# Kernel optimization log

Hardware: AMD Instinct MI355X
Metric: run time of the kernel (lower is better)

Reference implementation:

```python
import jax, jax.numpy as jnp
import numpy as np


def _pairwise_sq_dist(a, b):
    # a: (B,N,D), b: (B,M,D) -> (B,N,M) squared euclidean distances
    # matmul trick matching torch.cdist (clamped at 0 before implicit sqrt)
    a2 = jnp.sum(a * a, axis=-1)  # (B,N)
    b2 = jnp.sum(b * b, axis=-1)  # (B,M)
    ab = jnp.einsum('bnd,bmd->bnm', a, b)  # (B,N,M)
    d2 = a2[:, :, None] + b2[:, None, :] - 2.0 * ab
    return jnp.maximum(d2, 0.0)


def setup_inputs() -> dict:
    key = jax.random.key(0)
    k1, k2 = jax.random.split(key)
    B, N, M, D = 8, 8192, 8192, 3
    gts = jax.random.normal(k1, (B, N, D), dtype=jnp.float32)
    preds = jax.random.normal(k2, (B, M, D), dtype=jnp.float32)
    return {"gts": gts, "preds": preds}


def reference(gts, preds):
    d2 = _pairwise_sq_dist(gts, preds)           # (B,N,M)
    min_g2p = jnp.min(d2, axis=2)                # (B,N) nearest pred for each gt
    min_p2g = jnp.min(d2, axis=1)                # (B,M) nearest gt for each pred
    return jnp.mean(min_g2p) + jnp.mean(min_p2g)
```

## Files before the change

kernel.cpp:

```cpp
#include <hip/hip_runtime.h>
#include <math.h>

#define BB 8
#define NN 8192
#define MM 8192

#define ROWS_PER_BLOCK 256
#define COLS_PER_BLOCK 1024
#define NTILES (COLS_PER_BLOCK / 32)

typedef __attribute__((ext_vector_type(8)))  short short8;
typedef __attribute__((ext_vector_type(16))) float float16;

#define ONE_BF16 ((short)0x3F80)

__device__ inline unsigned short bf16rn(float f) {
    unsigned int u = __float_as_uint(f);
    u += 0x7FFFu + ((u >> 16) & 1u);
    return (unsigned short)(u >> 16);
}
__device__ inline float bf2f(unsigned short h) {
    return __uint_as_float(((unsigned int)h) << 16);
}
__device__ inline float min16(const float16 d) {
    float v = fminf(fminf(d[0], d[1]), d[2]);
    v = fminf(fminf(v, d[3]),  d[4]);
    v = fminf(fminf(v, d[5]),  d[6]);
    v = fminf(fminf(v, d[7]),  d[8]);
    v = fminf(fminf(v, d[9]),  d[10]);
    v = fminf(fminf(v, d[11]), d[12]);
    v = fminf(fminf(v, d[13]), d[14]);
    return fminf(v, d[15]);
}


__global__ __launch_bounds__(512, 4) void chamfer_main(
    const float* __restrict__ gts, const float* __restrict__ preds,
    unsigned int* __restrict__ minn, unsigned int* __restrict__ minp)
{
    __shared__ short8 sBlo[COLS_PER_BLOCK];
    __shared__ short8 sBhi[COLS_PER_BLOCK];
    __shared__ int colmin[COLS_PER_BLOCK];

    const int b       = blockIdx.z;
    const int rowBase = blockIdx.x * ROWS_PER_BLOCK;
    const int colBase = blockIdx.y * COLS_PER_BLOCK;
    const int tid  = threadIdx.x;
    const int lane = tid & 63;
    const int wave = tid >> 6;
    const int h    = lane >> 5;
    const int c    = lane & 31;

    for (int i = tid; i < COLS_PER_BLOCK; i += 512) {
        const float* p = preds + ((size_t)b * MM + colBase + i) * 3;
        float x = p[0], y = p[1], z = p[2];
        float w = x * x + y * y + z * z;
        unsigned short xh = bf16rn(x), yh = bf16rn(y), zh = bf16rn(z);
        unsigned short xl = bf16rn(x - bf2f(xh));
        unsigned short yl = bf16rn(y - bf2f(yh));
        unsigned short zl = bf16rn(z - bf2f(zh));
        unsigned short wh = bf16rn(w);
        unsigned short wl = bf16rn(w - bf2f(wh));
        short8 lo, hi;
        lo[0]=(short)xh; lo[1]=(short)yh; lo[2]=(short)zh; lo[3]=(short)xl;
        lo[4]=(short)yl; lo[5]=(short)zl; lo[6]=(short)xh; lo[7]=(short)yh;
        hi[0]=(short)zh; hi[1]=ONE_BF16;  hi[2]=ONE_BF16;  hi[3]=(short)wh;
        hi[4]=(short)wl; hi[5]=0;         hi[6]=0;         hi[7]=0;
        sBlo[i] = lo; sBhi[i] = hi;
        colmin[i] = 0x7F800000;
    }

    const float* g = gts + ((size_t)b * NN + rowBase + wave * 32 + c) * 3;
    float gx = g[0], gy = g[1], gz = g[2];
    float gw = gx * gx + gy * gy + gz * gz;
    float mx = -2.0f * gx, my = -2.0f * gy, mz = -2.0f * gz;
    unsigned short axh = bf16rn(mx), ayh = bf16rn(my), azh = bf16rn(mz);
    unsigned short axl = bf16rn(mx - bf2f(axh));
    unsigned short ayl = bf16rn(my - bf2f(ayh));
    unsigned short azl = bf16rn(mz - bf2f(azh));
    unsigned short awh = bf16rn(gw);
    unsigned short awl = bf16rn(gw - bf2f(awh));
    short8 alo, ahi;
    alo[0]=(short)axh; alo[1]=(short)ayh; alo[2]=(short)azh; alo[3]=(short)axh;
    alo[4]=(short)ayh; alo[5]=(short)azh; alo[6]=(short)axl; alo[7]=(short)ayl;
    ahi[0]=(short)azl; ahi[1]=(short)awh; ahi[2]=(short)awl; ahi[3]=ONE_BF16;
    ahi[4]=ONE_BF16;   ahi[5]=0;          ahi[6]=0;          ahi[7]=0;
    short8 afrag = h ? ahi : alo;

    float16 zacc;
#pragma unroll
    for (int q = 0; q < 16; ++q) zacc[q] = 0.0f;

    const float kInf = __builtin_inff();
    float rm[16];
#pragma unroll
    for (int q = 0; q < 16; ++q) rm[q] = kInf;

    __syncthreads();

    const short8* myB = h ? sBhi : sBlo;
    for (int t = 0; t < NTILES; t += 2) {
        short8 b0 = myB[t * 32 + c];
        short8 b1 = myB[(t + 1) * 32 + c];
        float16 d0 = __builtin_amdgcn_mfma_f32_32x32x16_bf16(afrag, b0, zacc, 0, 0, 0);
        float16 d1 = __builtin_amdgcn_mfma_f32_32x32x16_bf16(afrag, b1, zacc, 0, 0, 0);
        atomicMin(&colmin[t * 32 + c],       __float_as_int(min16(d0)));
        atomicMin(&colmin[(t + 1) * 32 + c], __float_as_int(min16(d1)));
#pragma unroll
        for (int q = 0; q < 16; ++q)
            rm[q] = fminf(fminf(rm[q], d0[q]), d1[q]);
    }

#pragma unroll
    for (int q = 0; q < 16; ++q) {
        float v = rm[q];
        v = fminf(v, __shfl_xor(v, 1));
        v = fminf(v, __shfl_xor(v, 2));
        v = fminf(v, __shfl_xor(v, 4));
        v = fminf(v, __shfl_xor(v, 8));
        v = fminf(v, __shfl_xor(v, 16));
        rm[q] = v;
    }
    float sel = rm[0];
#pragma unroll
    for (int q = 1; q < 16; ++q) sel = (c == q) ? rm[q] : sel;
    if (c < 16) {
        int rowInTile = (c & 3) + 8 * (c >> 2) + 4 * h;
        unsigned int bits = __float_as_uint(fmaxf(sel, 0.0f));
        atomicMin(&minn[(size_t)b * NN + rowBase + wave * 32 + rowInTile], bits);
    }

    __syncthreads();
    for (int i = tid; i < COLS_PER_BLOCK; i += 512) {
        unsigned int bits = __float_as_uint(fmaxf(__int_as_float(colmin[i]), 0.0f));
        atomicMin(&minp[(size_t)b * MM + colBase + i], bits);
    }
}

__global__ void chamfer_reduce(const unsigned int* __restrict__ minn,
                               const unsigned int* __restrict__ minp,
                               float* __restrict__ accum,
                               unsigned int* __restrict__ ticket,
                               float* __restrict__ out)
{
    const int idx = blockIdx.x * blockDim.x + threadIdx.x;
    const int stride = gridDim.x * blockDim.x;

    float s0 = 0.0f, s1 = 0.0f;
    for (int i = idx; i < BB * NN; i += stride) s0 += __uint_as_float(minn[i]);
    for (int i = idx; i < BB * MM; i += stride) s1 += __uint_as_float(minp[i]);

#pragma unroll
    for (int m = 1; m < 64; m <<= 1) {
        s0 += __shfl_xor(s0, m, 64);
        s1 += __shfl_xor(s1, m, 64);
    }
    __shared__ float w0[4], w1[4];
    if ((threadIdx.x & 63) == 0) {
        w0[threadIdx.x >> 6] = s0;
        w1[threadIdx.x >> 6] = s1;
    }
    __syncthreads();
    if (threadIdx.x == 0) {
        atomicAdd(&accum[0], w0[0] + w0[1] + w0[2] + w0[3]);
        atomicAdd(&accum[1], w1[0] + w1[1] + w1[2] + w1[3]);
        __threadfence();
        unsigned int old = atomicAdd(ticket, 1u);
        unsigned int G = gridDim.x;
        if (old == 0xAAAAAAAAu + G - 1u || old == G - 1u) {
            float a0 = atomicAdd(&accum[0], 0.0f);
            float a1 = atomicAdd(&accum[1], 0.0f);
            out[0] = a0 / (float)(BB * NN) + a1 / (float)(BB * MM);
        }
    }
}

extern "C" void kernel_launch(void* const* d_in, const int* in_sizes, int n_in,
                              void* d_out, int out_size, void* d_ws, size_t ws_size,
                              hipStream_t stream) {
    const float* gts   = (const float*)d_in[0];
    const float* preds = (const float*)d_in[1];
    float* out = (float*)d_out;

    unsigned int* minn   = (unsigned int*)d_ws;
    unsigned int* minp   = minn + (size_t)BB * NN;
    float*        accum  = (float*)(minp + (size_t)BB * MM);
    unsigned int* ticket = (unsigned int*)(accum + 2);

    dim3 grid(NN / ROWS_PER_BLOCK, MM / COLS_PER_BLOCK, BB);
    chamfer_main<<<grid, 512, 0, stream>>>(gts, preds, minn, minp);

    chamfer_reduce<<<64, 256, 0, stream>>>(minn, minp, accum, ticket, out);
}
```

Baseline: 93.80 us.

## Fuse chamfer into one kernel computing both directions as row-min passes

```diff
diff --git a/kernel.cpp b/kernel.cpp
--- a/kernel.cpp
+++ b/kernel.cpp
@@ -2,12 +2,7 @@
 #include <math.h>
 
 #define BB 8
-#define NN 8192
-#define MM 8192
-
-#define ROWS_PER_BLOCK 256
-#define COLS_PER_BLOCK 1024
-#define NTILES (COLS_PER_BLOCK / 32)
+#define PTS 8192
 
 typedef __attribute__((ext_vector_type(8)))  short short8;
 typedef __attribute__((ext_vector_type(16))) float float16;
@@ -22,155 +17,115 @@
 __device__ inline float bf2f(unsigned short h) {
     return __uint_as_float(((unsigned int)h) << 16);
 }
-__device__ inline float min16(const float16 d) {
-    float v = fminf(fminf(d[0], d[1]), d[2]);
-    v = fminf(fminf(v, d[3]),  d[4]);
-    v = fminf(fminf(v, d[5]),  d[6]);
-    v = fminf(fminf(v, d[7]),  d[8]);
-    v = fminf(fminf(v, d[9]),  d[10]);
-    v = fminf(fminf(v, d[11]), d[12]);
-    v = fminf(fminf(v, d[13]), d[14]);
-    return fminf(v, d[15]);
-}
 
+__global__ __launch_bounds__(512, 2) void chamfer_fused(
+    const float* __restrict__ gts, const float* __restrict__ preds,
+    float* __restrict__ accum, unsigned int* __restrict__ ticket,
+    float* __restrict__ out)
+{
+    __shared__ short8 sBlo[512];
+    __shared__ short8 sBhi[512];
 
-__global__ __launch_bounds__(512, 4) void chamfer_main(
-    const float* __restrict__ gts, const float* __restrict__ preds,
-    unsigned int* __restrict__ minn, unsigned int* __restrict__ minp)
-{
-    __shared__ short8 sBlo[COLS_PER_BLOCK];
-    __shared__ short8 sBhi[COLS_PER_BLOCK];
-    __shared__ int colmin[COLS_PER_BLOCK];
-
-    const int b       = blockIdx.z;
-    const int rowBase = blockIdx.x * ROWS_PER_BLOCK;
-    const int colBase = blockIdx.y * COLS_PER_BLOCK;
+    const int id     = blockIdx.x;
+    const int role   = id >> 8;
+    const int within = id & 255;
+    const int batch  = within >> 5;
+    const int qblk   = within & 31;
     const int tid  = threadIdx.x;
     const int lane = tid & 63;
     const int wave = tid >> 6;
     const int h    = lane >> 5;
     const int c    = lane & 31;
 
-    for (int i = tid; i < COLS_PER_BLOCK; i += 512) {
-        const float* p = preds + ((size_t)b * MM + colBase + i) * 3;
-        float x = p[0], y = p[1], z = p[2];
-        float w = x * x + y * y + z * z;
-        unsigned short xh = bf16rn(x), yh = bf16rn(y), zh = bf16rn(z);
-        unsigned short xl = bf16rn(x - bf2f(xh));
-        unsigned short yl = bf16rn(y - bf2f(yh));
-        unsigned short zl = bf16rn(z - bf2f(zh));
-        unsigned short wh = bf16rn(w);
-        unsigned short wl = bf16rn(w - bf2f(wh));
-        short8 lo, hi;
-        lo[0]=(short)xh; lo[1]=(short)yh; lo[2]=(short)zh; lo[3]=(short)xl;
-        lo[4]=(short)yl; lo[5]=(short)zl; lo[6]=(short)xh; lo[7]=(short)yh;
-        hi[0]=(short)zh; hi[1]=ONE_BF16;  hi[2]=ONE_BF16;  hi[3]=(short)wh;
-        hi[4]=(short)wl; hi[5]=0;         hi[6]=0;         hi[7]=0;
-        sBlo[i] = lo; sBhi[i] = hi;
-        colmin[i] = 0x7F800000;
-    }
+    const float* Q  = role ? preds : gts;
+    const float* DB = role ? gts : preds;
 
-    const float* g = gts + ((size_t)b * NN + rowBase + wave * 32 + c) * 3;
-    float gx = g[0], gy = g[1], gz = g[2];
-    float gw = gx * gx + gy * gy + gz * gz;
-    float mx = -2.0f * gx, my = -2.0f * gy, mz = -2.0f * gz;
-    unsigned short axh = bf16rn(mx), ayh = bf16rn(my), azh = bf16rn(mz);
-    unsigned short axl = bf16rn(mx - bf2f(axh));
-    unsigned short ayl = bf16rn(my - bf2f(ayh));
-    unsigned short azl = bf16rn(mz - bf2f(azh));
-    unsigned short awh = bf16rn(gw);
-    unsigned short awl = bf16rn(gw - bf2f(awh));
+    const float* q = Q + ((size_t)batch * PTS + qblk * 256 + wave * 32 + c) * 3;
+    float qx = q[0], qy = q[1], qz = q[2];
+    float wa = qx * qx + qy * qy + qz * qz;
+    float mX = -2.0f * qx, mY = -2.0f * qy, mZ = -2.0f * qz;
+    unsigned short mxh = bf16rn(mX), myh = bf16rn(mY), mzh = bf16rn(mZ);
+    unsigned short mxl = bf16rn(mX - bf2f(mxh));
+    unsigned short myl = bf16rn(mY - bf2f(myh));
+    unsigned short mzl = bf16rn(mZ - bf2f(mzh));
+    unsigned short awh = bf16rn(wa);
+    unsigned short awl = bf16rn(wa - bf2f(awh));
     short8 alo, ahi;
-    alo[0]=(short)axh; alo[1]=(short)ayh; alo[2]=(short)azh; alo[3]=(short)axh;
-    alo[4]=(short)ayh; alo[5]=(short)azh; alo[6]=(short)axl; alo[7]=(short)ayl;
-    ahi[0]=(short)azl; ahi[1]=(short)awh; ahi[2]=(short)awl; ahi[3]=ONE_BF16;
-    ahi[4]=ONE_BF16;   ahi[5]=0;          ahi[6]=0;          ahi[7]=0;
+    alo[0]=(short)mxh; alo[1]=(short)myh; alo[2]=(short)mzh; alo[3]=(short)mxh;
+    alo[4]=(short)myh; alo[5]=(short)mzh; alo[6]=(short)mxl; alo[7]=(short)myl;
+    ahi[0]=(short)mzl; ahi[1]=(short)mxl; ahi[2]=(short)myl; ahi[3]=(short)mzl;
+    ahi[4]=(short)awh; ahi[5]=(short)awl; ahi[6]=ONE_BF16;   ahi[7]=ONE_BF16;
     short8 afrag = h ? ahi : alo;
 
     float16 zacc;
 #pragma unroll
-    for (int q = 0; q < 16; ++q) zacc[q] = 0.0f;
+    for (int i = 0; i < 16; ++i) zacc[i] = 0.0f;
 
     const float kInf = __builtin_inff();
     float rm[16];
 #pragma unroll
-    for (int q = 0; q < 16; ++q) rm[q] = kInf;
+    for (int i = 0; i < 16; ++i) rm[i] = kInf;
 
-    __syncthreads();
+    const float* dbase = DB + (size_t)batch * PTS * 3;
 
-    const short8* myB = h ? sBhi : sBlo;
-    for (int t = 0; t < NTILES; t += 2) {
-        short8 b0 = myB[t * 32 + c];
-        short8 b1 = myB[(t + 1) * 32 + c];
-        float16 d0 = __builtin_amdgcn_mfma_f32_32x32x16_bf16(afrag, b0, zacc, 0, 0, 0);
-        float16 d1 = __builtin_amdgcn_mfma_f32_32x32x16_bf16(afrag, b1, zacc, 0, 0, 0);
-        atomicMin(&colmin[t * 32 + c],       __float_as_int(min16(d0)));
-        atomicMin(&colmin[(t + 1) * 32 + c], __float_as_int(min16(d1)));
+    for (int ch = 0; ch < PTS; ch += 512) {
+        __syncthreads();
+        {
+            const float* p = dbase + (size_t)(ch + tid) * 3;
+            float x = p[0], y = p[1], z = p[2];
+            float w = x * x + y * y + z * z;
+            unsigned short xh = bf16rn(x), yh = bf16rn(y), zh = bf16rn(z);
+            unsigned short xl = bf16rn(x - bf2f(xh));
+            unsigned short yl = bf16rn(y - bf2f(yh));
+            unsigned short zl = bf16rn(z - bf2f(zh));
+            unsigned short wh = bf16rn(w);
+            unsigned short wl = bf16rn(w - bf2f(wh));
+            short8 lo, hi;
+            lo[0]=(short)xh; lo[1]=(short)yh; lo[2]=(short)zh; lo[3]=(short)xl;
+            lo[4]=(short)yl; lo[5]=(short)zl; lo[6]=(short)xh; lo[7]=(short)yh;
+            hi[0]=(short)zh; hi[1]=(short)xl; hi[2]=(short)yl; hi[3]=(short)zl;
+            hi[4]=ONE_BF16;  hi[5]=ONE_BF16;  hi[6]=(short)wh; hi[7]=(short)wl;
+            sBlo[tid] = lo; sBhi[tid] = hi;
+        }
+        __syncthreads();
+
+        const short8* myB = h ? sBhi : sBlo;
 #pragma unroll
-        for (int q = 0; q < 16; ++q)
-            rm[q] = fminf(fminf(rm[q], d0[q]), d1[q]);
+        for (int t = 0; t < 16; t += 2) {
+            short8 b0 = myB[t * 32 + c];
+            short8 b1 = myB[t * 32 + 32 + c];
+            float16 d0 = __builtin_amdgcn_mfma_f32_32x32x16_bf16(afrag, b0, zacc, 0, 0, 0);
+            float16 d1 = __builtin_amdgcn_mfma_f32_32x32x16_bf16(afrag, b1, zacc, 0, 0, 0);
+#pragma unroll
+            for (int i = 0; i < 16; ++i)
+                rm[i] = fminf(fminf(rm[i], d0[i]), d1[i]);
+        }
     }
 
 #pragma unroll
-    for (int q = 0; q < 16; ++q) {
-        float v = rm[q];
+    for (int i = 0; i < 16; ++i) {
+        float v = rm[i];
         v = fminf(v, __shfl_xor(v, 1));
         v = fminf(v, __shfl_xor(v, 2));
         v = fminf(v, __shfl_xor(v, 4));
         v = fminf(v, __shfl_xor(v, 8));
         v = fminf(v, __shfl_xor(v, 16));
-        rm[q] = v;
+        rm[i] = v;
     }
-    float sel = rm[0];
+    float s = 0.0f;
 #pragma unroll
-    for (int q = 1; q < 16; ++q) sel = (c == q) ? rm[q] : sel;
-    if (c < 16) {
-        int rowInTile = (c & 3) + 8 * (c >> 2) + 4 * h;
-        unsigned int bits = __float_as_uint(fmaxf(sel, 0.0f));
-        atomicMin(&minn[(size_t)b * NN + rowBase + wave * 32 + rowInTile], bits);
-    }
+    for (int i = 0; i < 16; ++i) s += fmaxf(rm[i], 0.0f);
+    s += __shfl_xor(s, 32);
+    if (lane == 0) atomicAdd(accum, s);
 
     __syncthreads();
-    for (int i = tid; i < COLS_PER_BLOCK; i += 512) {
-        unsigned int bits = __float_as_uint(fmaxf(__int_as_float(colmin[i]), 0.0f));
-        atomicMin(&minp[(size_t)b * MM + colBase + i], bits);
-    }
-}
-
-__global__ void chamfer_reduce(const unsigned int* __restrict__ minn,
-                               const unsigned int* __restrict__ minp,
-                               float* __restrict__ accum,
-                               unsigned int* __restrict__ ticket,
-                               float* __restrict__ out)
-{
-    const int idx = blockIdx.x * blockDim.x + threadIdx.x;
-    const int stride = gridDim.x * blockDim.x;
-
-    float s0 = 0.0f, s1 = 0.0f;
-    for (int i = idx; i < BB * NN; i += stride) s0 += __uint_as_float(minn[i]);
-    for (int i = idx; i < BB * MM; i += stride) s1 += __uint_as_float(minp[i]);
-
-#pragma unroll
-    for (int m = 1; m < 64; m <<= 1) {
-        s0 += __shfl_xor(s0, m, 64);
-        s1 += __shfl_xor(s1, m, 64);
-    }
-    __shared__ float w0[4], w1[4];
-    if ((threadIdx.x & 63) == 0) {
-        w0[threadIdx.x >> 6] = s0;
-        w1[threadIdx.x >> 6] = s1;
-    }
-    __syncthreads();
-    if (threadIdx.x == 0) {
-        atomicAdd(&accum[0], w0[0] + w0[1] + w0[2] + w0[3]);
-        atomicAdd(&accum[1], w1[0] + w1[1] + w1[2] + w1[3]);
+    if (tid == 0) {
         __threadfence();
         unsigned int old = atomicAdd(ticket, 1u);
         unsigned int G = gridDim.x;
         if (old == 0xAAAAAAAAu + G - 1u || old == G - 1u) {
-            float a0 = atomicAdd(&accum[0], 0.0f);
-            float a1 = atomicAdd(&accum[1], 0.0f);
-            out[0] = a0 / (float)(BB * NN) + a1 / (float)(BB * MM);
+            float a = atomicAdd(accum, 0.0f);
+            out[0] = a / (float)(BB * PTS);
         }
     }
 }
@@ -182,13 +137,8 @@
     const float* preds = (const float*)d_in[1];
     float* out = (float*)d_out;
 
-    unsigned int* minn   = (unsigned int*)d_ws;
-    unsigned int* minp   = minn + (size_t)BB * NN;
-    float*        accum  = (float*)(minp + (size_t)BB * MM);
-    unsigned int* ticket = (unsigned int*)(accum + 2);
+    float*        accum  = (float*)d_ws;
+    unsigned int* ticket = (unsigned int*)d_ws + 1;
 
-    dim3 grid(NN / ROWS_PER_BLOCK, MM / COLS_PER_BLOCK, BB);
-    chamfer_main<<<grid, 512, 0, stream>>>(gts, preds, minn, minp);
-
-    chamfer_reduce<<<64, 256, 0, stream>>>(minn, minp, accum, ticket, out);
+    chamfer_fused<<<512, 512, 0, stream>>>(gts, preds, accum, ticket, out);
 }
```

Result: slower. 137.9 us (+47.1%).

## Give each wave a 64x64 register tile to halve LDS column atomics

Applied to the files above, without the earlier changes.

```diff
diff --git a/kernel.cpp b/kernel.cpp
--- a/kernel.cpp
+++ b/kernel.cpp
@@ -6,8 +6,8 @@
 #define MM 8192
 
 #define ROWS_PER_BLOCK 256
-#define COLS_PER_BLOCK 1024
-#define NTILES (COLS_PER_BLOCK / 32)
+#define COLS_PER_BLOCK 512
+#define NITER (COLS_PER_BLOCK / 64)
 
 typedef __attribute__((ext_vector_type(8)))  short short8;
 typedef __attribute__((ext_vector_type(16))) float float16;
@@ -22,19 +22,46 @@
 __device__ inline float bf2f(unsigned short h) {
     return __uint_as_float(((unsigned int)h) << 16);
 }
-__device__ inline float min16(const float16 d) {
-    float v = fminf(fminf(d[0], d[1]), d[2]);
-    v = fminf(fminf(v, d[3]),  d[4]);
-    v = fminf(fminf(v, d[5]),  d[6]);
-    v = fminf(fminf(v, d[7]),  d[8]);
-    v = fminf(fminf(v, d[9]),  d[10]);
-    v = fminf(fminf(v, d[11]), d[12]);
-    v = fminf(fminf(v, d[13]), d[14]);
-    return fminf(v, d[15]);
-}
-
-
-__global__ __launch_bounds__(512, 4) void chamfer_main(
+
+__device__ inline float tree32(const float16 a, const float16 b) {
+    float v = fminf(a[0], a[1]);
+    v = fminf(fminf(v, a[2]),  a[3]);
+    v = fminf(fminf(v, a[4]),  a[5]);
+    v = fminf(fminf(v, a[6]),  a[7]);
+    v = fminf(fminf(v, a[8]),  a[9]);
+    v = fminf(fminf(v, a[10]), a[11]);
+    v = fminf(fminf(v, a[12]), a[13]);
+    v = fminf(fminf(v, a[14]), a[15]);
+    v = fminf(fminf(v, b[0]),  b[1]);
+    v = fminf(fminf(v, b[2]),  b[3]);
+    v = fminf(fminf(v, b[4]),  b[5]);
+    v = fminf(fminf(v, b[6]),  b[7]);
+    v = fminf(fminf(v, b[8]),  b[9]);
+    v = fminf(fminf(v, b[10]), b[11]);
+    v = fminf(fminf(v, b[12]), b[13]);
+    v = fminf(fminf(v, b[14]), b[15]);
+    return v;
+}
+
+__device__ inline short8 make_afrag(const float* g, int h) {
+    float gx = g[0], gy = g[1], gz = g[2];
+    float gw = gx * gx + gy * gy + gz * gz;
+    float mx = -2.0f * gx, my = -2.0f * gy, mz = -2.0f * gz;
+    unsigned short axh = bf16rn(mx), ayh = bf16rn(my), azh = bf16rn(mz);
+    unsigned short axl = bf16rn(mx - bf2f(axh));
+    unsigned short ayl = bf16rn(my - bf2f(ayh));
+    unsigned short azl = bf16rn(mz - bf2f(azh));
+    unsigned short awh = bf16rn(gw);
+    unsigned short awl = bf16rn(gw - bf2f(awh));
+    short8 lo, hi;
+    lo[0]=(short)axh; lo[1]=(short)ayh; lo[2]=(short)azh; lo[3]=(short)axh;
+    lo[4]=(short)ayh; lo[5]=(short)azh; lo[6]=(short)axl; lo[7]=(short)ayl;
+    hi[0]=(short)azl; hi[1]=(short)awh; hi[2]=(short)awl; hi[3]=ONE_BF16;
+    hi[4]=ONE_BF16;   hi[5]=0;          hi[6]=0;          hi[7]=0;
+    return h ? hi : lo;
+}
+
+__global__ __launch_bounds__(256, 2) void chamfer_main(
     const float* __restrict__ gts, const float* __restrict__ preds,
     unsigned int* __restrict__ minn, unsigned int* __restrict__ minp)
 {
@@ -51,7 +78,7 @@
     const int h    = lane >> 5;
     const int c    = lane & 31;
 
-    for (int i = tid; i < COLS_PER_BLOCK; i += 512) {
+    for (int i = tid; i < COLS_PER_BLOCK; i += 256) {
         const float* p = preds + ((size_t)b * MM + colBase + i) * 3;
         float x = p[0], y = p[1], z = p[2];
         float w = x * x + y * y + z * z;
@@ -70,68 +97,64 @@
         colmin[i] = 0x7F800000;
     }
 
-    const float* g = gts + ((size_t)b * NN + rowBase + wave * 32 + c) * 3;
-    float gx = g[0], gy = g[1], gz = g[2];
-    float gw = gx * gx + gy * gy + gz * gz;
-    float mx = -2.0f * gx, my = -2.0f * gy, mz = -2.0f * gz;
-    unsigned short axh = bf16rn(mx), ayh = bf16rn(my), azh = bf16rn(mz);
-    unsigned short axl = bf16rn(mx - bf2f(axh));
-    unsigned short ayl = bf16rn(my - bf2f(ayh));
-    unsigned short azl = bf16rn(mz - bf2f(azh));
-    unsigned short awh = bf16rn(gw);
-    unsigned short awl = bf16rn(gw - bf2f(awh));
-    short8 alo, ahi;
-    alo[0]=(short)axh; alo[1]=(short)ayh; alo[2]=(short)azh; alo[3]=(short)axh;
-    alo[4]=(short)ayh; alo[5]=(short)azh; alo[6]=(short)axl; alo[7]=(short)ayl;
-    ahi[0]=(short)azl; ahi[1]=(short)awh; ahi[2]=(short)awl; ahi[3]=ONE_BF16;
-    ahi[4]=ONE_BF16;   ahi[5]=0;          ahi[6]=0;          ahi[7]=0;
-    short8 afrag = h ? ahi : alo;
+    const float* g0 = gts + ((size_t)b * NN + rowBase + wave * 64 + c) * 3;
+    short8 a0 = make_afrag(g0, h);
+    short8 a1 = make_afrag(g0 + 32 * 3, h);
 
     float16 zacc;
 #pragma unroll
     for (int q = 0; q < 16; ++q) zacc[q] = 0.0f;
 
     const float kInf = __builtin_inff();
-    float rm[16];
-#pragma unroll
-    for (int q = 0; q < 16; ++q) rm[q] = kInf;
+    float rm0[16], rm1[16];
+#pragma unroll
+    for (int q = 0; q < 16; ++q) { rm0[q] = kInf; rm1[q] = kInf; }
 
     __syncthreads();
 
     const short8* myB = h ? sBhi : sBlo;
-    for (int t = 0; t < NTILES; t += 2) {
-        short8 b0 = myB[t * 32 + c];
-        short8 b1 = myB[(t + 1) * 32 + c];
-        float16 d0 = __builtin_amdgcn_mfma_f32_32x32x16_bf16(afrag, b0, zacc, 0, 0, 0);
-        float16 d1 = __builtin_amdgcn_mfma_f32_32x32x16_bf16(afrag, b1, zacc, 0, 0, 0);
-        atomicMin(&colmin[t * 32 + c],       __float_as_int(min16(d0)));
-        atomicMin(&colmin[(t + 1) * 32 + c], __float_as_int(min16(d1)));
-#pragma unroll
-        for (int q = 0; q < 16; ++q)
-            rm[q] = fminf(fminf(rm[q], d0[q]), d1[q]);
-    }
-
+#pragma unroll 2
+    for (int j = 0; j < NITER; ++j) {
+        short8 b0 = myB[j * 64 + c];
+        short8 b1 = myB[j * 64 + 32 + c];
+        float16 d00 = __builtin_amdgcn_mfma_f32_32x32x16_bf16(a0, b0, zacc, 0, 0, 0);
+        float16 d10 = __builtin_amdgcn_mfma_f32_32x32x16_bf16(a1, b0, zacc, 0, 0, 0);
+        float16 d01 = __builtin_amdgcn_mfma_f32_32x32x16_bf16(a0, b1, zacc, 0, 0, 0);
+        float16 d11 = __builtin_amdgcn_mfma_f32_32x32x16_bf16(a1, b1, zacc, 0, 0, 0);
+#pragma unroll
+        for (int q = 0; q < 16; ++q) {
+            rm0[q] = fminf(fminf(rm0[q], d00[q]), d01[q]);
+            rm1[q] = fminf(fminf(rm1[q], d10[q]), d11[q]);
+        }
+        atomicMin(&colmin[j * 64 + c],      __float_as_int(tree32(d00, d10)));
+        atomicMin(&colmin[j * 64 + 32 + c], __float_as_int(tree32(d01, d11)));
+    }
+
+    unsigned int* rowDst0 = minn + (size_t)b * NN + rowBase + wave * 64;
 #pragma unroll
     for (int q = 0; q < 16; ++q) {
-        float v = rm[q];
-        v = fminf(v, __shfl_xor(v, 1));
-        v = fminf(v, __shfl_xor(v, 2));
-        v = fminf(v, __shfl_xor(v, 4));
-        v = fminf(v, __shfl_xor(v, 8));
-        v = fminf(v, __shfl_xor(v, 16));
-        rm[q] = v;
-    }
-    float sel = rm[0];
-#pragma unroll
-    for (int q = 1; q < 16; ++q) sel = (c == q) ? rm[q] : sel;
+        float v0 = rm0[q], v1 = rm1[q];
+        v0 = fminf(v0, __shfl_xor(v0, 1));  v1 = fminf(v1, __shfl_xor(v1, 1));
+        v0 = fminf(v0, __shfl_xor(v0, 2));  v1 = fminf(v1, __shfl_xor(v1, 2));
+        v0 = fminf(v0, __shfl_xor(v0, 4));  v1 = fminf(v1, __shfl_xor(v1, 4));
+        v0 = fminf(v0, __shfl_xor(v0, 8));  v1 = fminf(v1, __shfl_xor(v1, 8));
+        v0 = fminf(v0, __shfl_xor(v0, 16)); v1 = fminf(v1, __shfl_xor(v1, 16));
+        rm0[q] = v0; rm1[q] = v1;
+    }
+    float sel0 = rm0[0], sel1 = rm1[0];
+#pragma unroll
+    for (int q = 1; q < 16; ++q) {
+        sel0 = (c == q) ? rm0[q] : sel0;
+        sel1 = (c == q) ? rm1[q] : sel1;
+    }
     if (c < 16) {
         int rowInTile = (c & 3) + 8 * (c >> 2) + 4 * h;
-        unsigned int bits = __float_as_uint(fmaxf(sel, 0.0f));
-        atomicMin(&minn[(size_t)b * NN + rowBase + wave * 32 + rowInTile], bits);
+        atomicMin(&rowDst0[rowInTile],      __float_as_uint(fmaxf(sel0, 0.0f)));
+        atomicMin(&rowDst0[32 + rowInTile], __float_as_uint(fmaxf(sel1, 0.0f)));
     }
 
     __syncthreads();
-    for (int i = tid; i < COLS_PER_BLOCK; i += 512) {
+    for (int i = tid; i < COLS_PER_BLOCK; i += 256) {
         unsigned int bits = __float_as_uint(fmaxf(__int_as_float(colmin[i]), 0.0f));
         atomicMin(&minp[(size_t)b * MM + colBase + i], bits);
     }
@@ -188,7 +211,7 @@
     unsigned int* ticket = (unsigned int*)(accum + 2);
 
     dim3 grid(NN / ROWS_PER_BLOCK, MM / COLS_PER_BLOCK, BB);
-    chamfer_main<<<grid, 512, 0, stream>>>(gts, preds, minn, minp);
+    chamfer_main<<<grid, 256, 0, stream>>>(gts, preds, minn, minp);
 
     chamfer_reduce<<<64, 256, 0, stream>>>(minn, minp, accum, ticket, out);
 }
```

Result: slower. 101.8 us (+8.5%).
